# Kernel optimization log

Measured on AMD Instinct MI355X. Metric: run time of the kernel, lower is better.

The kernel has to match this reference:

```python
import jax, jax.numpy as jnp
import numpy as np
from jax.scipy.special import logsumexp

NUM_JOINT_TYPES = 17
SINKHORN_ITERS = 30
SINKHORN_TAU = 0.05
BIG_COST = 1.0e6


def _scot_forward(embeddings, W1, b1, prototype_pool, joint_types, k):
    n = embeddings.shape[0]
    # node encoder: Linear + SELU
    h = jax.nn.selu(embeddings @ W1 + b1)  # [N, H]
    prototypes = prototype_pool[:k]        # [K, H] (k <= k_max)
    # squared euclidean distance (torch.cdist(p=2).pow(2))
    d2 = (jnp.sum(h * h, axis=1)[:, None]
          + jnp.sum(prototypes * prototypes, axis=1)[None, :]
          - 2.0 * (h @ prototypes.T))
    d2 = jnp.maximum(d2, 0.0)              # [N, K]
    # expand each person slot to 17 joint-type slots
    cost = jnp.repeat(d2, NUM_JOINT_TYPES, axis=1)          # [N, K*17]
    slot_types = jnp.tile(jnp.arange(NUM_JOINT_TYPES), k)   # [K*17]
    type_mask = joint_types[:, None] == slot_types[None, :]  # [N, K*17]
    cost = jnp.where(type_mask, cost, BIG_COST)

    n_slots = k * NUM_JOINT_TYPES
    log_K = -cost / SINKHORN_TAU
    log_K_ext = jnp.concatenate([log_K, jnp.zeros((n, 1), log_K.dtype)], axis=1)  # [N, K*17+1]
    # target marginal: 1 per slot, slack column absorbs leftover mass
    tm = jnp.ones(n_slots + 1, log_K.dtype).at[-1].set(float(max(n - n_slots, 1)))
    log_tm = jnp.log(tm)

    def step(carry, _):
        log_u, log_v = carry
        log_u = -logsumexp(log_K_ext + log_v[None, :], axis=1)   # row normalization
        log_v = log_tm - logsumexp(log_K_ext + log_u[:, None], axis=0)  # col normalization
        return (log_u, log_v), None

    init = (jnp.zeros(n, log_K.dtype), jnp.zeros(n_slots + 1, log_K.dtype))
    (log_u, log_v), _ = jax.lax.scan(step, init, None, length=SINKHORN_ITERS)

    T = jnp.exp(log_K_ext + log_u[:, None] + log_v[None, :])[:, :n_slots]  # [N, K*17]
    logits = jnp.log(T.reshape(n, k, NUM_JOINT_TYPES).sum(axis=2) + 1e-8)  # [N, K]
    return logits, T


def setup_inputs() -> dict:
    key = jax.random.key(0)
    k_emb, k_w, k_proto, k_jt = jax.random.split(key, 4)
    N, D, H, KMAX = 6144, 256, 256, 512
    emb = jax.random.normal(k_emb, (N, D), dtype=jnp.float32)
    emb = emb / jnp.linalg.norm(emb, axis=1, keepdims=True)  # L2-normalised per docstring
    W1 = jax.random.normal(k_w, (D, H), dtype=jnp.float32) * (1.0 / np.sqrt(D))
    b1 = jnp.zeros((H,), jnp.float32)
    prototype_pool = jax.random.normal(k_proto, (KMAX, H), dtype=jnp.float32) * 0.5
    joint_types = jax.random.randint(k_jt, (N,), 0, NUM_JOINT_TYPES)
    return {"embeddings": emb, "W1": W1, "b1": b1,
            "prototype_pool": prototype_pool, "joint_types": joint_types, "k": 300}


def reference(embeddings, W1, b1, prototype_pool, joint_types, k):
    return _scot_forward(embeddings, W1, b1, prototype_pool, joint_types, k)
```

## Files before the change

### kernel.cpp

```cpp
#include <hip/hip_runtime.h>
#include <math.h>

#define NT 17
#define NBLK 34
#define KCAP 300
#define KP 320
#define LCAP 208
#define CH 2
#define NITER 30
#define MSCALE2 28.853900817779268f

typedef unsigned long long u64;
typedef float vfloat4 __attribute__((ext_vector_type(4)));

#define EX2(x) __builtin_amdgcn_exp2f(x)
#define LG2(x) __builtin_amdgcn_logf(x)
#if __has_builtin(__builtin_amdgcn_rcpf)
#define RCP(x) __builtin_amdgcn_rcpf(x)
#else
#define RCP(x) (1.0f / (x))
#endif

__device__ inline unsigned bf16rne(float x) {
  unsigned u = __float_as_uint(x);
  return (u + 0x7FFFu + ((u >> 16) & 1u)) >> 16;
}
__device__ inline unsigned bfp(float lo, float hi) {
  return bf16rne(lo) | (bf16rne(hi) << 16);
}
#define BFLO(p) __uint_as_float((p) << 16)
#define BFHI(p) __uint_as_float((p) & 0xFFFF0000u)


__device__ inline float selu_f(float x) {
  const float scale = 1.0507009873554804934193349852946f;
  const float alpha = 1.6732632423543772848170429916717f;
  return x > 0.f ? scale * x : scale * alpha * (EX2(x * 1.4426950408889634f) - 1.f);
}

__global__ __launch_bounds__(1024) void k_bucket(const int* __restrict__ jt, int n,
    int* __restrict__ meta, int* __restrict__ perm, int* __restrict__ tys) {
  __shared__ int hist[NT];
  __shared__ int off[NT];
  __shared__ int cnt[NT];
  int tid = threadIdx.x;
  if (tid < NT) { hist[tid] = 0; cnt[tid] = 0; }
  __syncthreads();
  for (int i = tid; i < n; i += 1024) atomicAdd(&hist[jt[i]], 1);
  __syncthreads();
  if (tid == 0) {
    int o = 0;
    for (int t = 0; t < NT; t++) {
      off[t] = o; meta[32 + t] = o; meta[t] = hist[t]; o += hist[t];
    }
  }
  __syncthreads();
  for (int i = tid; i < n; i += 1024) {
    int t = jt[i];
    int pos = off[t] + atomicAdd(&cnt[t], 1);
    perm[pos] = i;
    tys[pos] = t;
  }
}

__global__ __launch_bounds__(256) void k_hgemm(const float* __restrict__ A,
    const float* __restrict__ B, const float* __restrict__ bias,
    float* __restrict__ C, int n, int D, int H) {
  __shared__ __align__(16) float As[16][68];
  __shared__ __align__(16) float Bs[16][68];
  int tid = threadIdx.x;
  int i0 = blockIdx.x * 64, j0 = blockIdx.y * 64;
  int tx = tid & 15, ty = tid >> 4;
  int aI = tid & 63, aK = (tid >> 6) << 2;
  int bJ = (tid & 15) << 2, bK = tid >> 4;
  float acc[4][4] = {};
  for (int k0 = 0; k0 < D; k0 += 16) {
    float4 av = *(const float4*)(A + (size_t)(i0 + aI) * D + k0 + aK);
    float4 bv = *(const float4*)(B + (size_t)(k0 + bK) * H + j0 + bJ);
    __syncthreads();
    As[aK + 0][aI] = av.x; As[aK + 1][aI] = av.y; As[aK + 2][aI] = av.z; As[aK + 3][aI] = av.w;
    *(float4*)(&Bs[bK][bJ]) = bv;
    __syncthreads();
#pragma unroll
    for (int kk = 0; kk < 16; kk++) {
      float4 a4 = *(float4*)(&As[kk][ty << 2]);
      float4 b4 = *(float4*)(&Bs[kk][tx << 2]);
      float aa[4] = {a4.x, a4.y, a4.z, a4.w};
      float bb[4] = {b4.x, b4.y, b4.z, b4.w};
#pragma unroll
      for (int p = 0; p < 4; p++)
#pragma unroll
        for (int q = 0; q < 4; q++)
          acc[p][q] = fmaf(aa[p], bb[q], acc[p][q]);
    }
  }
#pragma unroll
  for (int p = 0; p < 4; p++) {
    int i = i0 + (ty << 2) + p;
    float o[4];
#pragma unroll
    for (int q = 0; q < 4; q++) {
      int j = j0 + (tx << 2) + q;
      o[q] = selu_f(acc[p][q] + bias[j]);
    }
    *(float4*)(C + (size_t)i * H + j0 + (tx << 2)) = make_float4(o[0], o[1], o[2], o[3]);
  }
}

__global__ __launch_bounds__(256) void k_msort(const float* __restrict__ h,
    const float* __restrict__ P, const int* __restrict__ perm,
    float* __restrict__ Ms, int n, int H, int k) {
  __shared__ __align__(16) float As[16][68];
  __shared__ __align__(16) float Bs[16][68];
  __shared__ float hp[4][64];
  __shared__ float pp[4][64];
  __shared__ int gIdx[64];
  int tid = threadIdx.x;
  int i0 = blockIdx.x * 64, j0 = blockIdx.y * 64;
  if (tid < 64) gIdx[tid] = perm[i0 + tid];
  __syncthreads();
  int tx = tid & 15, ty = tid >> 4;
  int aI = tid & 63, aK = (tid >> 6) << 2;
  int gA = gIdx[aI];
  bool bok = (j0 + aI) < k;
  const float* bRow = P + (size_t)(j0 + (bok ? aI : 0)) * H;
  float acc[4][4] = {};
  float ha = 0.f, pa = 0.f;
  for (int k0 = 0; k0 < H; k0 += 16) {
    float4 av = *(const float4*)(h + (size_t)gA * H + k0 + aK);
    float4 bv = *(const float4*)(bRow + k0 + aK);
    ha += av.x * av.x + av.y * av.y + av.z * av.z + av.w * av.w;
    pa += bv.x * bv.x + bv.y * bv.y + bv.z * bv.z + bv.w * bv.w;
    __syncthreads();
    As[aK + 0][aI] = av.x; As[aK + 1][aI] = av.y; As[aK + 2][aI] = av.z; As[aK + 3][aI] = av.w;
    Bs[aK + 0][aI] = bv.x; Bs[aK + 1][aI] = bv.y; Bs[aK + 2][aI] = bv.z; Bs[aK + 3][aI] = bv.w;
    __syncthreads();
#pragma unroll
    for (int kk = 0; kk < 16; kk++) {
      float4 a4 = *(float4*)(&As[kk][ty << 2]);
      float4 b4 = *(float4*)(&Bs[kk][tx << 2]);
      float aa[4] = {a4.x, a4.y, a4.z, a4.w};
      float bb[4] = {b4.x, b4.y, b4.z, b4.w};
#pragma unroll
      for (int p = 0; p < 4; p++)
#pragma unroll
        for (int q = 0; q < 4; q++)
          acc[p][q] = fmaf(aa[p], bb[q], acc[p][q]);
    }
  }
  int grp = tid >> 6;
  hp[grp][aI] = ha;
  pp[grp][aI] = pa;
  __syncthreads();
#pragma unroll
  for (int p = 0; p < 4; p++) {
    int rr = (ty << 2) + p;
    int r = i0 + rr;
    float hq = hp[0][rr] + hp[1][rr] + hp[2][rr] + hp[3][rr];
#pragma unroll
    for (int q = 0; q < 4; q++) {
      int jl = (tx << 2) + q;
      int j = j0 + jl;
      if (j < k) {
        float pq = pp[0][jl] + pp[1][jl] + pp[2][jl] + pp[3][jl];
        float d2 = hq + pq - 2.f * acc[p][q];
        d2 = fmaxf(d2, 0.f);
        Ms[(size_t)r * k + j] = -d2 * MSCALE2;
      }
    }
  }
}

__global__ __launch_bounds__(1024) void k_sink(const float* __restrict__ Ms,
    unsigned short* __restrict__ Ms2, const int* __restrict__ meta,
    float* __restrict__ cmD, unsigned* __restrict__ cmE,
    float* __restrict__ pcD, unsigned* __restrict__ pcE,
    float* __restrict__ suD, unsigned* __restrict__ suE,
    float* __restrict__ uF, float* __restrict__ vF,
    int k, float tm_last) {
  __shared__ __align__(16) unsigned short Klds[LCAP * KP];
  __shared__ __align__(16) float WP2[16][KP];
  __shared__ __align__(16) float V[KP];
  __shared__ __align__(16) float Sown[KP];
  __shared__ float SU[16];
  __shared__ float w_sh;
  __shared__ int lvl_ep;
  __shared__ int pairflag;
  int tid = threadIdx.x, lane = tid & 63, wv = tid >> 6;
  int c = blockIdx.x;
  int t = c >> 1, hb = c & 1, prt = c ^ 1;
  int cRt = meta[t];
  int s0t = meta[32 + t];
  int h0 = (cRt + 1) >> 1;
  int rb = hb ? h0 : 0;
  int re = hb ? cRt : h0;
  int myR = re - rb;
  int s0 = s0t + rb;
  int ntH = (myR + 3) >> 2;
  bool l2v = (lane + 64) < (k >> 2);
  int g = lane >> 4, cg = lane & 15;
  bool r2a = (cg < 8);

  if (tid == 0) { w_sh = 1.f; lvl_ep = 0; pairflag = 0; }

  {
    float4 cm0 = make_float4(-3e38f, -3e38f, -3e38f, -3e38f);
    float4 cm1 = cm0;
    for (int tile = wv; tile < ntH; tile += 16) {
      int r0 = tile * 4;
#pragma unroll
      for (int rr = 0; rr < 4; rr++) {
        int rc = (r0 + rr < myR) ? (r0 + rr) : r0;
        const float4* rp = (const float4*)(Ms + (size_t)(s0 + rc) * k);
        float4 a0 = rp[lane];
        cm0.x = fmaxf(cm0.x, a0.x); cm0.y = fmaxf(cm0.y, a0.y);
        cm0.z = fmaxf(cm0.z, a0.z); cm0.w = fmaxf(cm0.w, a0.w);
        if (l2v) {
          float4 a1 = rp[lane + 64];
          cm1.x = fmaxf(cm1.x, a1.x); cm1.y = fmaxf(cm1.y, a1.y);
          cm1.z = fmaxf(cm1.z, a1.z); cm1.w = fmaxf(cm1.w, a1.w);
        }
      }
    }
    *(float4*)&WP2[wv][4 * lane] = cm0;
    if (l2v) *(float4*)&WP2[wv][4 * (lane + 64)] = cm1;
    __syncthreads();
    if (tid < k) {
      float cmax = WP2[0][tid];
#pragma unroll
      for (int q = 1; q < 16; q++) cmax = fmaxf(cmax, WP2[q][tid]);
      Sown[tid] = cmax;
      __hip_atomic_store(&cmD[c * KP + tid], cmax,
                         __ATOMIC_RELAXED, __HIP_MEMORY_SCOPE_AGENT);
    }
    __syncthreads();
    if (tid == 0) {
      __hip_atomic_store(&cmE[c * 16], 1u, __ATOMIC_RELAXED, __HIP_MEMORY_SCOPE_AGENT);
      while (__hip_atomic_load(&cmE[prt * 16], __ATOMIC_RELAXED, __HIP_MEMORY_SCOPE_AGENT) < 1u)
        __builtin_amdgcn_s_sleep(1);
      __hip_atomic_store(&pairflag, 1, __ATOMIC_RELEASE, __HIP_MEMORY_SCOPE_WORKGROUP);
    }
    if (tid < k) {
      while (__hip_atomic_load(&pairflag, __ATOMIC_ACQUIRE, __HIP_MEMORY_SCOPE_WORKGROUP) < 1)
        __builtin_amdgcn_s_sleep(1);
      float o = __hip_atomic_load(&cmD[prt * KP + tid],
                                  __ATOMIC_RELAXED, __HIP_MEMORY_SCOPE_AGENT);
      V[tid] = fmaxf(Sown[tid], o);
    }
    __syncthreads();
    float4 cx0 = *(const float4*)&V[4 * lane];
    float4 cx1 = l2v ? *(const float4*)&V[4 * (lane + 64)] : cx0;
    for (int tile = wv; tile < ntH; tile += 16) {
      int r0 = tile * 4;
#pragma unroll
      for (int rr = 0; rr < 4; rr++) {
        int r = r0 + rr;
        if (r < myR) {
          const float4* rp = (const float4*)(Ms + (size_t)(s0 + r) * k);
          char* orow = (char*)Ms2 + (size_t)(s0 + r) * (KP * 2);
          char* lrow = (char*)Klds + (size_t)r * (KP * 2);
          bool inL = (r < LCAP);
          float4 a0 = rp[lane];
          uint2 o;
          o.x = bfp(EX2(a0.x - cx0.x), EX2(a0.y - cx0.y));
          o.y = bfp(EX2(a0.z - cx0.z), EX2(a0.w - cx0.w));
          *(uint2*)(orow + 8 * lane) = o;
          if (inL) *(uint2*)(lrow + 8 * lane) = o;
          if (l2v) {
            float4 a1 = rp[lane + 64];
            uint2 o1;
            o1.x = bfp(EX2(a1.x - cx1.x), EX2(a1.y - cx1.y));
            o1.y = bfp(EX2(a1.z - cx1.z), EX2(a1.w - cx1.w));
            *(uint2*)(orow + 512 + 8 * lane) = o1;
            if (inL) *(uint2*)(lrow + 512 + 8 * lane) = o1;
          } else if (lane < 16) {
            *(uint2*)(orow + 512 + 8 * lane) = make_uint2(0u, 0u);
            if (inL) *(uint2*)(lrow + 512 + 8 * lane) = make_uint2(0u, 0u);
          }
        }
      }
    }
  }
  __syncthreads();
  if (tid < KP) V[tid] = 0.f;
  __syncthreads();

  for (int m = 0; m < NITER; m++) {
    int epoch = m + 1;
    int slot = m & 3;
    if (wv == 15) {
      if (m > 0) {
        int pslot = (m - 1) & 3;
        unsigned want = (unsigned)m;
        bool need = lane < NBLK;
        for (;;) {
          bool ok = !need ||
              (__hip_atomic_load(&suE[(pslot * NBLK + lane) * 16],
                                 __ATOMIC_RELAXED, __HIP_MEMORY_SCOPE_AGENT) >= want);
          if (__all(ok)) break;
          __builtin_amdgcn_s_sleep(1);
        }
        float s = need
            ? __hip_atomic_load(&suD[(pslot * NBLK + lane) * 16],
                                __ATOMIC_RELAXED, __HIP_MEMORY_SCOPE_AGENT)
            : 0.f;
#pragma unroll
        for (int o = 32; o; o >>= 1) s += __shfl_xor(s, o);
        if (lane == 0) w_sh = tm_last / s;
      }
      if (lane == 0)
        __hip_atomic_store(&lvl_ep, epoch, __ATOMIC_RELEASE, __HIP_MEMORY_SCOPE_WORKGROUP);
    }
    float w = 0.f;
    bool haveW = (wv == 15);
    float su = 0.f;
    float vv[3][8];
#pragma unroll
    for (int q3 = 0; q3 < 3; q3++) {
      if (q3 < 2 || r2a) {
        float4 x0 = *(const float4*)&V[q3 * 128 + cg * 8];
        float4 x1 = *(const float4*)&V[q3 * 128 + cg * 8 + 4];
        vv[q3][0] = x0.x; vv[q3][1] = x0.y; vv[q3][2] = x0.z; vv[q3][3] = x0.w;
        vv[q3][4] = x1.x; vv[q3][5] = x1.y; vv[q3][6] = x1.z; vv[q3][7] = x1.w;
      } else {
#pragma unroll
        for (int e = 0; e < 8; e++) vv[q3][e] = 0.f;
      }
    }
    float acc[3][8];
#pragma unroll
    for (int q3 = 0; q3 < 3; q3++)
#pragma unroll
      for (int e = 0; e < 8; e++) acc[q3][e] = 0.f;

    int t0 = (wv < 15) ? wv : ntH;
    for (; t0 < ntH; t0 += 15 * CH) {
      uint4 T[CH][3];
      float rs[CH];
#pragma unroll
      for (int ccc = 0; ccc < CH; ccc++) {
        int tile = t0 + 15 * ccc;
        rs[ccc] = 0.f;
        if (tile < ntH) {
          int r = tile * 4 + g;
          int rc = (r < myR) ? r : (myR - 1);
          uint4 z4 = make_uint4(0u, 0u, 0u, 0u);
          if (rc < LCAP) {
            const uint4* lp = (const uint4*)((const char*)Klds +
                (size_t)rc * (KP * 2) + (cg << 4));
            T[ccc][0] = lp[0];
            T[ccc][1] = lp[16];
            if (r2a) T[ccc][2] = lp[32]; else T[ccc][2] = z4;
          } else {
            const uint4* gp = (const uint4*)((const char*)Ms2 +
                (size_t)(s0 + rc) * (KP * 2) + (cg << 4));
            T[ccc][0] = gp[0];
            T[ccc][1] = gp[16];
            if (r2a) T[ccc][2] = gp[32]; else T[ccc][2] = z4;
          }
          float r1 = 0.f;
#pragma unroll
          for (int q3 = 0; q3 < 3; q3++) {
            r1 = fmaf(BFLO(T[ccc][q3].x), vv[q3][0], r1);
            r1 = fmaf(BFHI(T[ccc][q3].x), vv[q3][1], r1);
            r1 = fmaf(BFLO(T[ccc][q3].y), vv[q3][2], r1);
            r1 = fmaf(BFHI(T[ccc][q3].y), vv[q3][3], r1);
            r1 = fmaf(BFLO(T[ccc][q3].z), vv[q3][4], r1);
            r1 = fmaf(BFHI(T[ccc][q3].z), vv[q3][5], r1);
            r1 = fmaf(BFLO(T[ccc][q3].w), vv[q3][6], r1);
            r1 = fmaf(BFHI(T[ccc][q3].w), vv[q3][7], r1);
          }
          r1 += __shfl_xor(r1, 1); r1 += __shfl_xor(r1, 2);
          r1 += __shfl_xor(r1, 4); r1 += __shfl_xor(r1, 8);
          rs[ccc] = r1;
        }
      }
      if (!haveW) {
        while (__hip_atomic_load(&lvl_ep, __ATOMIC_ACQUIRE, __HIP_MEMORY_SCOPE_WORKGROUP) < epoch)
          __builtin_amdgcn_s_sleep(1);
        w = w_sh;
        haveW = true;
      }
#pragma unroll
      for (int ccc = 0; ccc < CH; ccc++) {
        int tile = t0 + 15 * ccc;
        if (tile < ntH) {
          int r = tile * 4 + g;
          bool valid = (r < myR);
          float u = RCP(rs[ccc] + w);
          float uu = valid ? u : 0.f;
          if (cg == 0) {
            su += uu;
            if (valid && m == NITER - 1) uF[s0 + r] = u;
          }
#pragma unroll
          for (int q3 = 0; q3 < 3; q3++) {
            acc[q3][0] = fmaf(BFLO(T[ccc][q3].x), uu, acc[q3][0]);
            acc[q3][1] = fmaf(BFHI(T[ccc][q3].x), uu, acc[q3][1]);
            acc[q3][2] = fmaf(BFLO(T[ccc][q3].y), uu, acc[q3][2]);
            acc[q3][3] = fmaf(BFHI(T[ccc][q3].y), uu, acc[q3][3]);
            acc[q3][4] = fmaf(BFLO(T[ccc][q3].z), uu, acc[q3][4]);
            acc[q3][5] = fmaf(BFHI(T[ccc][q3].z), uu, acc[q3][5]);
            acc[q3][6] = fmaf(BFLO(T[ccc][q3].w), uu, acc[q3][6]);
            acc[q3][7] = fmaf(BFHI(T[ccc][q3].w), uu, acc[q3][7]);
          }
        }
      }
    }
    if (!haveW) {
      while (__hip_atomic_load(&lvl_ep, __ATOMIC_ACQUIRE, __HIP_MEMORY_SCOPE_WORKGROUP) < epoch)
        __builtin_amdgcn_s_sleep(1);
      haveW = true;
    }

    if (wv < 15) {
#pragma unroll
      for (int q3 = 0; q3 < 3; q3++)
#pragma unroll
        for (int e = 0; e < 8; e++) {
          float a = acc[q3][e];
          a += __shfl_xor(a, 16);
          a += __shfl_xor(a, 32);
          acc[q3][e] = a;
        }
      if (lane < 16) {
#pragma unroll
        for (int q3 = 0; q3 < 3; q3++) {
          if (q3 < 2 || lane < 8) {
            *(float4*)&WP2[wv][q3 * 128 + lane * 8] =
                make_float4(acc[q3][0], acc[q3][1], acc[q3][2], acc[q3][3]);
            *(float4*)&WP2[wv][q3 * 128 + lane * 8 + 4] =
                make_float4(acc[q3][4], acc[q3][5], acc[q3][6], acc[q3][7]);
          }
        }
      }
      float sr = su;
      sr += __shfl_xor(sr, 16);
      sr += __shfl_xor(sr, 32);
      if (lane == 0) SU[wv] = sr;
    }
    __syncthreads();
    if (tid < k) {
      float s = WP2[0][tid];
#pragma unroll
      for (int q = 1; q < 15; q++) s += WP2[q][tid];
      Sown[tid] = s;
      __hip_atomic_store(&pcD[(slot * NBLK + c) * KP + tid], s,
                         __ATOMIC_RELAXED, __HIP_MEMORY_SCOPE_AGENT);
    }
    if (wv == 15) {
      float sp = (lane < 15) ? SU[lane] : 0.f;
#pragma unroll
      for (int o = 32; o; o >>= 1) sp += __shfl_xor(sp, o);
      if (lane == 0)
        __hip_atomic_store(&suD[(slot * NBLK + c) * 16], sp,
                           __ATOMIC_RELAXED, __HIP_MEMORY_SCOPE_AGENT);
      __builtin_amdgcn_s_waitcnt(0);
      if (lane == 0)
        __hip_atomic_store(&suE[(slot * NBLK + c) * 16], (unsigned)epoch,
                           __ATOMIC_RELAXED, __HIP_MEMORY_SCOPE_AGENT);
    }
    __syncthreads();
    if (tid == 0) {
      __hip_atomic_store(&pcE[(slot * NBLK + c) * 16], (unsigned)epoch,
                         __ATOMIC_RELAXED, __HIP_MEMORY_SCOPE_AGENT);
      while (__hip_atomic_load(&pcE[(slot * NBLK + prt) * 16],
                               __ATOMIC_RELAXED, __HIP_MEMORY_SCOPE_AGENT) < (unsigned)epoch)
        __builtin_amdgcn_s_sleep(1);
      __hip_atomic_store(&pairflag, m + 2, __ATOMIC_RELEASE, __HIP_MEMORY_SCOPE_WORKGROUP);
    }
    if (tid < k) {
      while (__hip_atomic_load(&pairflag, __ATOMIC_ACQUIRE, __HIP_MEMORY_SCOPE_WORKGROUP) < m + 2)
        __builtin_amdgcn_s_sleep(1);
      float sp = __hip_atomic_load(&pcD[(slot * NBLK + prt) * KP + tid],
                                   __ATOMIC_RELAXED, __HIP_MEMORY_SCOPE_AGENT);
      V[tid] = RCP(Sown[tid] + sp);
    }
    __syncthreads();
  }
  if (hb == 0)
    for (int j = tid; j < k; j += 1024) vF[(size_t)t * k + j] = V[j];
}

__global__ __launch_bounds__(256) void k_epi(const unsigned short* __restrict__ Ms2,
    const float* __restrict__ uF, const float* __restrict__ vF,
    const int* __restrict__ perm, const int* __restrict__ tys,
    float* __restrict__ out, int n, int k) {
  __shared__ float vals[KCAP];
  int r = blockIdx.x;
  int i = perm[r], t = tys[r];
  float u = uF[r];
  const unsigned short* Krow = Ms2 + (size_t)r * KP;
  const float* Vrow = vF + (size_t)t * k;
  for (int j = threadIdx.x; j < k; j += 256)
    vals[j] = __uint_as_float((unsigned)Krow[j] << 16) * u * Vrow[j];
  __syncthreads();
  float* lg = out + (size_t)i * k;
  for (int j = threadIdx.x; j < k; j += 256)
    __builtin_nontemporal_store(LG2(vals[j] + 1e-8f) * 0.6931471805599453f, &lg[j]);
  int ns = k * NT;
  float* Trow = out + (size_t)n * k + (size_t)i * ns;
  if ((ns & 3) == 0) {
    int n4 = ns >> 2;
    int o0 = threadIdx.x << 2;
    int rmod = o0 % NT;
    for (int g4 = threadIdx.x; g4 < n4; g4 += 256, o0 += 1024) {
      int sstar = t - rmod; if (sstar < 0) sstar += NT;
      int j = (unsigned)(o0 + sstar) / (unsigned)NT;
      float vv = vals[j < k ? j : 0];
      vfloat4 v;
      v.x = (sstar == 0) ? vv : 0.f;
      v.y = (sstar == 1) ? vv : 0.f;
      v.z = (sstar == 2) ? vv : 0.f;
      v.w = (sstar == 3) ? vv : 0.f;
      __builtin_nontemporal_store(v, (vfloat4*)(Trow + o0));
      rmod += 4; if (rmod >= NT) rmod -= NT;
    }
  } else {
    for (int o = threadIdx.x; o < ns; o += 256) {
      int j = o / NT;
      int tt = o - j * NT;
      Trow[o] = (tt == t) ? vals[j] : 0.f;
    }
  }
}

extern "C" void kernel_launch(void* const* d_in, const int* in_sizes, int n_in,
                              void* d_out, int out_size, void* d_ws, size_t ws_size,
                              hipStream_t stream) {
  const float* emb = (const float*)d_in[0];
  const float* W1  = (const float*)d_in[1];
  const float* b1  = (const float*)d_in[2];
  const float* P   = (const float*)d_in[3];
  const int*   jt  = (const int*)d_in[4];
  (void)n_in; (void)ws_size;

  const int n = in_sizes[4];
  const int H = in_sizes[2];
  const int D = in_sizes[1] / H;
  const int k = out_size / (n * (NT + 1));
  const int nslots = k * NT;
  const float tm_last = (float)((n - nslots) > 1 ? (n - nslots) : 1);

  char* w = (char*)d_ws;
  size_t off = 0;
  auto take = [&](size_t bytes) -> char* {
    char* p = w + off;
    off = (off + bytes + 255) & ~(size_t)255;
    return p;
  };
  int*      meta = (int*)take(4096);
  int*      perm = (int*)take((size_t)n * 4);
  int*      tys  = (int*)take((size_t)n * 4);
  float*    h    = (float*)take((size_t)n * H * 4);
  float*    Ms   = (float*)take((size_t)n * k * 4);
  unsigned short* Ms2 = (unsigned short*)take((size_t)n * KP * 2 + 1024);
  float*    cmD  = (float*)take((size_t)NBLK * KP * 4);
  unsigned* cmE  = (unsigned*)take((size_t)NBLK * 64);
  float*    pcD  = (float*)take((size_t)4 * NBLK * KP * 4);
  unsigned* pcE  = (unsigned*)take((size_t)4 * NBLK * 64);
  float*    suD  = (float*)take((size_t)4 * NBLK * 64);
  unsigned* suE  = (unsigned*)take((size_t)4 * NBLK * 64);
  float*    uF   = (float*)take((size_t)n * 4);
  float*    vF   = (float*)take((size_t)NT * k * 4);

  (void)hipMemsetAsync(cmE, 0, (size_t)NBLK * 64, stream);
  (void)hipMemsetAsync(pcE, 0, (size_t)4 * NBLK * 64, stream);
  (void)hipMemsetAsync(suE, 0, (size_t)4 * NBLK * 64, stream);
  k_bucket<<<1, 1024, 0, stream>>>(jt, n, meta, perm, tys);
  k_hgemm<<<dim3(n / 64, H / 64), dim3(256), 0, stream>>>(emb, W1, b1, h, n, D, H);
  k_msort<<<dim3(n / 64, (k + 63) / 64), dim3(256), 0, stream>>>(h, P, perm, Ms, n, H, k);
  k_sink<<<NBLK, 1024, 0, stream>>>(Ms, Ms2, meta, cmD, cmE, pcD, pcE,
                                    suD, suE, uF, vF, k, tm_last);
  k_epi<<<n, 256, 0, stream>>>(Ms2, uF, vF, perm, tys, (float*)d_out, n, k);
}
```

Measured before the change: 424.1 us.

## Run Sinkhorn with one block per joint type, removing pairwise cross-block exchange

```diff
diff --git a/kernel.cpp b/kernel.cpp
--- a/kernel.cpp
+++ b/kernel.cpp
@@ -2,9 +2,10 @@
 #include <math.h>
 
 #define NT 17
-#define NBLK 34
+#define NB 17
 #define KCAP 300
 #define KP 320
+#define LROW 656
 #define LCAP 208
 #define CH 2
 #define NITER 30
@@ -173,40 +174,30 @@
 
 __global__ __launch_bounds__(1024) void k_sink(const float* __restrict__ Ms,
     unsigned short* __restrict__ Ms2, const int* __restrict__ meta,
-    float* __restrict__ cmD, unsigned* __restrict__ cmE,
-    float* __restrict__ pcD, unsigned* __restrict__ pcE,
     float* __restrict__ suD, unsigned* __restrict__ suE,
     float* __restrict__ uF, float* __restrict__ vF,
     int k, float tm_last) {
-  __shared__ __align__(16) unsigned short Klds[LCAP * KP];
-  __shared__ __align__(16) float WP2[16][KP];
+  __shared__ __align__(16) char Klds[LCAP * LROW];
+  __shared__ __align__(16) float WP2[15][KP];
   __shared__ __align__(16) float V[KP];
-  __shared__ __align__(16) float Sown[KP];
-  __shared__ float SU[16];
+  __shared__ float SU[15];
   __shared__ float w_sh;
   __shared__ int lvl_ep;
-  __shared__ int pairflag;
   int tid = threadIdx.x, lane = tid & 63, wv = tid >> 6;
-  int c = blockIdx.x;
-  int t = c >> 1, hb = c & 1, prt = c ^ 1;
-  int cRt = meta[t];
-  int s0t = meta[32 + t];
-  int h0 = (cRt + 1) >> 1;
-  int rb = hb ? h0 : 0;
-  int re = hb ? cRt : h0;
-  int myR = re - rb;
-  int s0 = s0t + rb;
-  int ntH = (myR + 3) >> 2;
+  int t = blockIdx.x;
+  int myR = meta[t];
+  int s0 = meta[32 + t];
+  int ntF = (myR + 3) >> 2;
   bool l2v = (lane + 64) < (k >> 2);
   int g = lane >> 4, cg = lane & 15;
   bool r2a = (cg < 8);
 
-  if (tid == 0) { w_sh = 1.f; lvl_ep = 0; pairflag = 0; }
-
-  {
+  if (tid == 0) { w_sh = 1.f; lvl_ep = 0; }
+
+  if (wv < 15) {
     float4 cm0 = make_float4(-3e38f, -3e38f, -3e38f, -3e38f);
     float4 cm1 = cm0;
-    for (int tile = wv; tile < ntH; tile += 16) {
+    for (int tile = wv; tile < ntF; tile += 15) {
       int r0 = tile * 4;
 #pragma unroll
       for (int rr = 0; rr < 4; rr++) {
@@ -224,33 +215,19 @@
     }
     *(float4*)&WP2[wv][4 * lane] = cm0;
     if (l2v) *(float4*)&WP2[wv][4 * (lane + 64)] = cm1;
-    __syncthreads();
-    if (tid < k) {
-      float cmax = WP2[0][tid];
-#pragma unroll
-      for (int q = 1; q < 16; q++) cmax = fmaxf(cmax, WP2[q][tid]);
-      Sown[tid] = cmax;
-      __hip_atomic_store(&cmD[c * KP + tid], cmax,
-                         __ATOMIC_RELAXED, __HIP_MEMORY_SCOPE_AGENT);
-    }
-    __syncthreads();
-    if (tid == 0) {
-      __hip_atomic_store(&cmE[c * 16], 1u, __ATOMIC_RELAXED, __HIP_MEMORY_SCOPE_AGENT);
-      while (__hip_atomic_load(&cmE[prt * 16], __ATOMIC_RELAXED, __HIP_MEMORY_SCOPE_AGENT) < 1u)
-        __builtin_amdgcn_s_sleep(1);
-      __hip_atomic_store(&pairflag, 1, __ATOMIC_RELEASE, __HIP_MEMORY_SCOPE_WORKGROUP);
-    }
-    if (tid < k) {
-      while (__hip_atomic_load(&pairflag, __ATOMIC_ACQUIRE, __HIP_MEMORY_SCOPE_WORKGROUP) < 1)
-        __builtin_amdgcn_s_sleep(1);
-      float o = __hip_atomic_load(&cmD[prt * KP + tid],
-                                  __ATOMIC_RELAXED, __HIP_MEMORY_SCOPE_AGENT);
-      V[tid] = fmaxf(Sown[tid], o);
-    }
-    __syncthreads();
+  }
+  __syncthreads();
+  if (tid < k) {
+    float cmax = WP2[0][tid];
+#pragma unroll
+    for (int q = 1; q < 15; q++) cmax = fmaxf(cmax, WP2[q][tid]);
+    V[tid] = cmax;
+  }
+  __syncthreads();
+  {
     float4 cx0 = *(const float4*)&V[4 * lane];
     float4 cx1 = l2v ? *(const float4*)&V[4 * (lane + 64)] : cx0;
-    for (int tile = wv; tile < ntH; tile += 16) {
+    for (int tile = wv; tile < ntF; tile += 16) {
       int r0 = tile * 4;
 #pragma unroll
       for (int rr = 0; rr < 4; rr++) {
@@ -258,7 +235,7 @@
         if (r < myR) {
           const float4* rp = (const float4*)(Ms + (size_t)(s0 + r) * k);
           char* orow = (char*)Ms2 + (size_t)(s0 + r) * (KP * 2);
-          char* lrow = (char*)Klds + (size_t)r * (KP * 2);
+          char* lrow = Klds + (size_t)r * LROW;
           bool inL = (r < LCAP);
           float4 a0 = rp[lane];
           uint2 o;
@@ -292,16 +269,16 @@
       if (m > 0) {
         int pslot = (m - 1) & 3;
         unsigned want = (unsigned)m;
-        bool need = lane < NBLK;
+        bool need = lane < NB;
         for (;;) {
           bool ok = !need ||
-              (__hip_atomic_load(&suE[(pslot * NBLK + lane) * 16],
+              (__hip_atomic_load(&suE[(pslot * NB + lane) * 16],
                                  __ATOMIC_RELAXED, __HIP_MEMORY_SCOPE_AGENT) >= want);
           if (__all(ok)) break;
           __builtin_amdgcn_s_sleep(1);
         }
         float s = need
-            ? __hip_atomic_load(&suD[(pslot * NBLK + lane) * 16],
+            ? __hip_atomic_load(&suD[(pslot * NB + lane) * 16],
                                 __ATOMIC_RELAXED, __HIP_MEMORY_SCOPE_AGENT)
             : 0.f;
 #pragma unroll
@@ -333,21 +310,20 @@
 #pragma unroll
       for (int e = 0; e < 8; e++) acc[q3][e] = 0.f;
 
-    int t0 = (wv < 15) ? wv : ntH;
-    for (; t0 < ntH; t0 += 15 * CH) {
+    int t0 = (wv < 15) ? wv : ntF;
+    for (; t0 < ntF; t0 += 15 * CH) {
       uint4 T[CH][3];
       float rs[CH];
 #pragma unroll
       for (int ccc = 0; ccc < CH; ccc++) {
         int tile = t0 + 15 * ccc;
         rs[ccc] = 0.f;
-        if (tile < ntH) {
+        if (tile < ntF) {
           int r = tile * 4 + g;
           int rc = (r < myR) ? r : (myR - 1);
           uint4 z4 = make_uint4(0u, 0u, 0u, 0u);
           if (rc < LCAP) {
-            const uint4* lp = (const uint4*)((const char*)Klds +
-                (size_t)rc * (KP * 2) + (cg << 4));
+            const uint4* lp = (const uint4*)(Klds + (size_t)rc * LROW + (cg << 4));
             T[ccc][0] = lp[0];
             T[ccc][1] = lp[16];
             if (r2a) T[ccc][2] = lp[32]; else T[ccc][2] = z4;
@@ -384,7 +360,7 @@
 #pragma unroll
       for (int ccc = 0; ccc < CH; ccc++) {
         int tile = t0 + 15 * ccc;
-        if (tile < ntH) {
+        if (tile < ntF) {
           int r = tile * 4 + g;
           bool valid = (r < myR);
           float u = RCP(rs[ccc] + w);
@@ -440,46 +416,27 @@
       if (lane == 0) SU[wv] = sr;
     }
     __syncthreads();
-    if (tid < k) {
+    if (tid < KP) {
       float s = WP2[0][tid];
 #pragma unroll
       for (int q = 1; q < 15; q++) s += WP2[q][tid];
-      Sown[tid] = s;
-      __hip_atomic_store(&pcD[(slot * NBLK + c) * KP + tid], s,
-                         __ATOMIC_RELAXED, __HIP_MEMORY_SCOPE_AGENT);
+      V[tid] = (tid < k) ? RCP(s) : 0.f;
     }
     if (wv == 15) {
       float sp = (lane < 15) ? SU[lane] : 0.f;
 #pragma unroll
       for (int o = 32; o; o >>= 1) sp += __shfl_xor(sp, o);
       if (lane == 0)
-        __hip_atomic_store(&suD[(slot * NBLK + c) * 16], sp,
+        __hip_atomic_store(&suD[(slot * NB + t) * 16], sp,
                            __ATOMIC_RELAXED, __HIP_MEMORY_SCOPE_AGENT);
       __builtin_amdgcn_s_waitcnt(0);
       if (lane == 0)
-        __hip_atomic_store(&suE[(slot * NBLK + c) * 16], (unsigned)epoch,
+        __hip_atomic_store(&suE[(slot * NB + t) * 16], (unsigned)epoch,
                            __ATOMIC_RELAXED, __HIP_MEMORY_SCOPE_AGENT);
     }
     __syncthreads();
-    if (tid == 0) {
-      __hip_atomic_store(&pcE[(slot * NBLK + c) * 16], (unsigned)epoch,
-                         __ATOMIC_RELAXED, __HIP_MEMORY_SCOPE_AGENT);
-      while (__hip_atomic_load(&pcE[(slot * NBLK + prt) * 16],
-                               __ATOMIC_RELAXED, __HIP_MEMORY_SCOPE_AGENT) < (unsigned)epoch)
-        __builtin_amdgcn_s_sleep(1);
-      __hip_atomic_store(&pairflag, m + 2, __ATOMIC_RELEASE, __HIP_MEMORY_SCOPE_WORKGROUP);
-    }
-    if (tid < k) {
-      while (__hip_atomic_load(&pairflag, __ATOMIC_ACQUIRE, __HIP_MEMORY_SCOPE_WORKGROUP) < m + 2)
-        __builtin_amdgcn_s_sleep(1);
-      float sp = __hip_atomic_load(&pcD[(slot * NBLK + prt) * KP + tid],
-                                   __ATOMIC_RELAXED, __HIP_MEMORY_SCOPE_AGENT);
-      V[tid] = RCP(Sown[tid] + sp);
-    }
-    __syncthreads();
-  }
-  if (hb == 0)
-    for (int j = tid; j < k; j += 1024) vF[(size_t)t * k + j] = V[j];
+  }
+  for (int j = tid; j < k; j += 1024) vF[(size_t)t * k + j] = V[j];
 }
 
 __global__ __launch_bounds__(256) void k_epi(const unsigned short* __restrict__ Ms2,
@@ -555,22 +512,15 @@
   float*    h    = (float*)take((size_t)n * H * 4);
   float*    Ms   = (float*)take((size_t)n * k * 4);
   unsigned short* Ms2 = (unsigned short*)take((size_t)n * KP * 2 + 1024);
-  float*    cmD  = (float*)take((size_t)NBLK * KP * 4);
-  unsigned* cmE  = (unsigned*)take((size_t)NBLK * 64);
-  float*    pcD  = (float*)take((size_t)4 * NBLK * KP * 4);
-  unsigned* pcE  = (unsigned*)take((size_t)4 * NBLK * 64);
-  float*    suD  = (float*)take((size_t)4 * NBLK * 64);
-  unsigned* suE  = (unsigned*)take((size_t)4 * NBLK * 64);
+  float*    suD  = (float*)take((size_t)4 * NB * 64);
+  unsigned* suE  = (unsigned*)take((size_t)4 * NB * 64);
   float*    uF   = (float*)take((size_t)n * 4);
   float*    vF   = (float*)take((size_t)NT * k * 4);
 
-  (void)hipMemsetAsync(cmE, 0, (size_t)NBLK * 64, stream);
-  (void)hipMemsetAsync(pcE, 0, (size_t)4 * NBLK * 64, stream);
-  (void)hipMemsetAsync(suE, 0, (size_t)4 * NBLK * 64, stream);
+  (void)hipMemsetAsync(suE, 0, (size_t)4 * NB * 64, stream);
   k_bucket<<<1, 1024, 0, stream>>>(jt, n, meta, perm, tys);
   k_hgemm<<<dim3(n / 64, H / 64), dim3(256), 0, stream>>>(emb, W1, b1, h, n, D, H);
   k_msort<<<dim3(n / 64, (k + 63) / 64), dim3(256), 0, stream>>>(h, P, perm, Ms, n, H, k);
-  k_sink<<<NBLK, 1024, 0, stream>>>(Ms, Ms2, meta, cmD, cmE, pcD, pcE,
-                                    suD, suE, uF, vF, k, tm_last);
+  k_sink<<<NB, 1024, 0, stream>>>(Ms, Ms2, meta, suD, suE, uF, vF, k, tm_last);
   k_epi<<<n, 256, 0, stream>>>(Ms2, uF, vF, perm, tys, (float*)d_out, n, k);
 }
```

New measurement: 459.8 us. 1.08x slower.
